# Kernel optimization log

Hardware: AMD Instinct MI355X
Metric: run time of the kernel (lower is better)

## Reference

```python
import jax, jax.numpy as jnp
import numpy as np

BATCH = 256
INPUT_DIM = 64
LEVELS = 100
HV_DIM = 10000


def setup_inputs() -> dict:
    key = jax.random.key(0)
    kx, kb = jax.random.split(key)
    x = jax.random.uniform(kx, (BATCH, INPUT_DIM), dtype=jnp.float32)
    base = jax.random.normal(kb, (INPUT_DIM, LEVELS, HV_DIM), dtype=jnp.float32)
    # buffer is L2-normalized along hv_dim at construction time
    base = base / jnp.linalg.norm(base, axis=-1, keepdims=True)
    return {"x": x, "base_hvs": base}


def reference(x, base_hvs):
    D, L, H = base_hvs.shape
    B = x.shape[0]
    xn = jnp.clip(x * (L - 1), 0.0, float(L - 1))          # [B, D]
    lo = jnp.floor(xn).astype(jnp.int32)                    # [B, D]
    hi = jnp.clip(lo + 1, 0, L - 1)                         # [B, D]
    alpha = xn - lo.astype(x.dtype)                         # [B, D]

    def step(acc, inputs):
        bhv, l, h, a = inputs    # bhv: [L, H], l/h/a: [B]
        hv_low = bhv[l]          # [B, H] gather
        hv_high = bhv[h]         # [B, H] gather
        a = a[:, None]
        return acc + (1.0 - a) * hv_low + a * hv_high, None

    init = jnp.zeros((B, H), dtype=x.dtype)
    encoded, _ = jax.lax.scan(step, init, (base_hvs, lo.T, hi.T, alpha.T))
    return encoded / jnp.linalg.norm(encoded, axis=-1, keepdims=True)
```

## Files before the change

### kernel.cpp

```cpp
#include <hip/hip_runtime.h>
#include <hip/hip_fp16.h>

#define BATCH   256
#define DIMS    64
#define LEVELS  100
#define HVD     10000
#define WH      128
#define NHT     79
#define DSPLIT  8
#define DPER    8
#define TPB     512

__global__ __launch_bounds__(TPB, 4) void encode_kernel(
    const float* __restrict__ x,
    const float* __restrict__ base,
    float* __restrict__ partial)
{
    __shared__ float    s_chunk[LEVELS * WH];
    __shared__ unsigned s_prm[DPER][BATCH];

    const int tid   = threadIdx.x;
    const int w     = tid >> 6;
    const int lane  = tid & 63;
    const int htile = blockIdx.x;
    const int split = blockIdx.y;
    const int h0    = htile * WH;
    const int d0    = split * DPER;
    const int wvalid = (HVD - h0) < WH ? (HVD - h0) : WH;

    for (int i = tid; i < DPER * BATCH; i += TPB) {
        const int dl = i >> 8;
        const int b  = i & 255;
        float xv = x[b * DIMS + d0 + dl];
        float xn = fminf(fmaxf(xv * (float)(LEVELS - 1), 0.0f), (float)(LEVELS - 1));
        float fl = floorf(xn);
        int   lo = (int)fl;
        int   hi = lo < LEVELS - 1 ? lo + 1 : LEVELS - 1;
        unsigned abits = (unsigned)__half_as_ushort(__float2half(xn - fl));
        s_prm[dl][b] = abits | ((unsigned)lo << 16) | ((unsigned)hi << 24);
    }

    const int cix   = lane * 2;
    const int bbase = w * 32;
    const int srow  = lane >> 5;
    const int scol  = (lane & 31) * 4;

    float2 acc[32];
    #pragma unroll
    for (int j = 0; j < 32; ++j) acc[j] = make_float2(0.f, 0.f);

    #pragma unroll 1
    for (int dc = 0; dc < DPER; ++dc) {
        __syncthreads();

        const float* src = base + ((size_t)(d0 + dc) * LEVELS) * (size_t)HVD + h0;
        for (int p = w; p < LEVELS / 2; p += 8) {
            const float* g = src + (size_t)(2 * p + srow) * HVD + scol;
            if (scol < wvalid) {
                __builtin_amdgcn_global_load_lds(
                    (const __attribute__((address_space(1))) unsigned*)g,
                    (__attribute__((address_space(3))) unsigned*)&s_chunk[p * 2 * WH],
                    16, 0, 0);
            }
        }
        __syncthreads();

        #pragma unroll
        for (int jj = 0; jj < 16; ++jj) {
            uint2 pr = *(const uint2*)&s_prm[dc][bbase + 2 * jj];
            {
                const unsigned pk = pr.x;
                const float a  = __half2float(__ushort_as_half((unsigned short)(pk & 0xffffu)));
                const int olo  = (int)((pk >> 16) & 0xffu) * WH;
                const int ohi  = (int)(pk >> 24) * WH;
                float2 vlo = *(const float2*)&s_chunk[olo + cix];
                float2 vhi = *(const float2*)&s_chunk[ohi + cix];
                const float wl = 1.0f - a;
                acc[2 * jj].x += wl * vlo.x + a * vhi.x;
                acc[2 * jj].y += wl * vlo.y + a * vhi.y;
            }
            {
                const unsigned pk = pr.y;
                const float a  = __half2float(__ushort_as_half((unsigned short)(pk & 0xffffu)));
                const int olo  = (int)((pk >> 16) & 0xffu) * WH;
                const int ohi  = (int)(pk >> 24) * WH;
                float2 vlo = *(const float2*)&s_chunk[olo + cix];
                float2 vhi = *(const float2*)&s_chunk[ohi + cix];
                const float wl = 1.0f - a;
                acc[2 * jj + 1].x += wl * vlo.x + a * vhi.x;
                acc[2 * jj + 1].y += wl * vlo.y + a * vhi.y;
            }
        }
    }

    if (cix < wvalid) {
        float* dst = partial + ((size_t)split * BATCH) * (size_t)HVD + h0 + cix;
        #pragma unroll
        for (int j = 0; j < 32; ++j)
            *(float2*)(dst + (size_t)(bbase + j) * HVD) = acc[j];
    }
}

__global__ __launch_bounds__(256) void finish_kernel(
    const float* __restrict__ partial,
    float* __restrict__ out)
{
    const int b   = blockIdx.x;
    const int tid = threadIdx.x;

    float ss = 0.f;
    for (int i = tid; i < HVD / 4; i += 256) {
        float4 s = make_float4(0.f, 0.f, 0.f, 0.f);
        #pragma unroll
        for (int sp = 0; sp < DSPLIT; ++sp) {
            const float4 v = *(const float4*)(partial +
                ((size_t)sp * BATCH + b) * (size_t)HVD + i * 4);
            s.x += v.x; s.y += v.y; s.z += v.z; s.w += v.w;
        }
        *(float4*)(out + (size_t)b * HVD + i * 4) = s;
        ss += s.x * s.x + s.y * s.y + s.z * s.z + s.w * s.w;
    }

    __shared__ float red[256];
    red[tid] = ss;
    __syncthreads();
    #pragma unroll
    for (int s = 128; s > 0; s >>= 1) {
        if (tid < s) red[tid] += red[tid + s];
        __syncthreads();
    }
    const float inv = rsqrtf(red[0]);

    for (int i = tid; i < HVD / 4; i += 256) {
        float4 v = *(float4*)(out + (size_t)b * HVD + i * 4);
        v.x *= inv; v.y *= inv; v.z *= inv; v.w *= inv;
        *(float4*)(out + (size_t)b * HVD + i * 4) = v;
    }
}

extern "C" void kernel_launch(void* const* d_in, const int* in_sizes, int n_in,
                              void* d_out, int out_size, void* d_ws, size_t ws_size,
                              hipStream_t stream)
{
    const float* x    = (const float*)d_in[0];
    const float* base = (const float*)d_in[1];
    float*       out  = (float*)d_out;
    float*       part = (float*)d_ws;

    dim3 grid(NHT, DSPLIT);
    encode_kernel<<<grid, TPB, 0, stream>>>(x, base, part);
    finish_kernel<<<BATCH, 256, 0, stream>>>(part, out);
}
```

Measured before the change: 393.1 us.

## Store partials as bf16, precompute byte-offset params, widen LDS reads to float4

A separate setup kernel now computes the per-(dim,batch) lo/hi byte offsets and fp32 alpha once, and the encoder reads them from global memory instead of rebuilding them in shared memory in every block. Each lane now handles four columns for half as many batch rows, so each LDS read is a float4 (two batches per wave), and the per-split partial sums are written as bf16. This halves both the partial write traffic and the read traffic in the finish kernel. It costs an extra kernel launch and loses precision in the partial sums to bf16 rounding before the final reduction.

```diff
diff --git a/kernel.cpp b/kernel.cpp
--- a/kernel.cpp
+++ b/kernel.cpp
@@ -1,5 +1,5 @@
 #include <hip/hip_runtime.h>
-#include <hip/hip_fp16.h>
+#include <hip/hip_bf16.h>
 
 #define BATCH   256
 #define DIMS    64
@@ -11,13 +11,38 @@
 #define DPER    8
 #define TPB     512
 
+typedef unsigned int  uint;
+typedef unsigned short ushort;
+
+#define PRM_OFF_BYTES (DSPLIT * BATCH * HVD * 2)
+
+static __device__ __forceinline__ ushort f2bf(float f) {
+    __hip_bfloat16 h = __float2bfloat16(f);
+    return *reinterpret_cast<ushort*>(&h);
+}
+
+__global__ __launch_bounds__(256) void setup_kernel(
+    const float* __restrict__ x, uint2* __restrict__ prm)
+{
+    const int i = blockIdx.x * 256 + threadIdx.x;
+    if (i >= DIMS * BATCH) return;
+    const int d = i >> 8;
+    const int b = i & 255;
+    float xv = x[b * DIMS + d];
+    float xn = fminf(fmaxf(xv * (float)(LEVELS - 1), 0.0f), (float)(LEVELS - 1));
+    float fl = floorf(xn);
+    int   lo = (int)fl;
+    int   hi = lo < LEVELS - 1 ? lo + 1 : LEVELS - 1;
+    prm[i] = make_uint2((uint)(lo * WH * 4) | ((uint)(hi * WH * 4) << 16),
+                        __float_as_uint(xn - fl));
+}
+
 __global__ __launch_bounds__(TPB, 4) void encode_kernel(
-    const float* __restrict__ x,
     const float* __restrict__ base,
-    float* __restrict__ partial)
+    const uint2* __restrict__ prm,
+    ushort*      __restrict__ partial)
 {
-    __shared__ float    s_chunk[LEVELS * WH];
-    __shared__ unsigned s_prm[DPER][BATCH];
+    __shared__ float s_chunk[LEVELS * WH];
 
     const int tid   = threadIdx.x;
     const int w     = tid >> 6;
@@ -28,26 +53,19 @@
     const int d0    = split * DPER;
     const int wvalid = (HVD - h0) < WH ? (HVD - h0) : WH;
 
-    for (int i = tid; i < DPER * BATCH; i += TPB) {
-        const int dl = i >> 8;
-        const int b  = i & 255;
-        float xv = x[b * DIMS + d0 + dl];
-        float xn = fminf(fmaxf(xv * (float)(LEVELS - 1), 0.0f), (float)(LEVELS - 1));
-        float fl = floorf(xn);
-        int   lo = (int)fl;
-        int   hi = lo < LEVELS - 1 ? lo + 1 : LEVELS - 1;
-        unsigned abits = (unsigned)__half_as_ushort(__float2half(xn - fl));
-        s_prm[dl][b] = abits | ((unsigned)lo << 16) | ((unsigned)hi << 24);
-    }
+    const int wu    = __builtin_amdgcn_readfirstlane(w);
+    const int bbase = wu * 32;
 
-    const int cix   = lane * 2;
-    const int bbase = w * 32;
-    const int srow  = lane >> 5;
-    const int scol  = (lane & 31) * 4;
+    const int s   = lane >> 5;
+    const int c   = lane & 31;
+    const int cb  = c * 16;
+    const int c4  = c * 4;
+    const int srow = lane >> 5;
+    const int scol = (lane & 31) * 4;
 
-    float2 acc[32];
+    float4 acc[16];
     #pragma unroll
-    for (int j = 0; j < 32; ++j) acc[j] = make_float2(0.f, 0.f);
+    for (int j = 0; j < 16; ++j) acc[j] = make_float4(0.f, 0.f, 0.f, 0.f);
 
     #pragma unroll 1
     for (int dc = 0; dc < DPER; ++dc) {
@@ -58,51 +76,46 @@
             const float* g = src + (size_t)(2 * p + srow) * HVD + scol;
             if (scol < wvalid) {
                 __builtin_amdgcn_global_load_lds(
-                    (const __attribute__((address_space(1))) unsigned*)g,
-                    (__attribute__((address_space(3))) unsigned*)&s_chunk[p * 2 * WH],
+                    (const __attribute__((address_space(1))) uint*)g,
+                    (__attribute__((address_space(3))) uint*)&s_chunk[p * 2 * WH],
                     16, 0, 0);
             }
         }
         __syncthreads();
 
+        const uint2* pr = prm + (size_t)(d0 + dc) * BATCH + bbase;
+
         #pragma unroll
         for (int jj = 0; jj < 16; ++jj) {
-            uint2 pr = *(const uint2*)&s_prm[dc][bbase + 2 * jj];
-            {
-                const unsigned pk = pr.x;
-                const float a  = __half2float(__ushort_as_half((unsigned short)(pk & 0xffffu)));
-                const int olo  = (int)((pk >> 16) & 0xffu) * WH;
-                const int ohi  = (int)(pk >> 24) * WH;
-                float2 vlo = *(const float2*)&s_chunk[olo + cix];
-                float2 vhi = *(const float2*)&s_chunk[ohi + cix];
-                const float wl = 1.0f - a;
-                acc[2 * jj].x += wl * vlo.x + a * vhi.x;
-                acc[2 * jj].y += wl * vlo.y + a * vhi.y;
-            }
-            {
-                const unsigned pk = pr.y;
-                const float a  = __half2float(__ushort_as_half((unsigned short)(pk & 0xffffu)));
-                const int olo  = (int)((pk >> 16) & 0xffu) * WH;
-                const int ohi  = (int)(pk >> 24) * WH;
-                float2 vlo = *(const float2*)&s_chunk[olo + cix];
-                float2 vhi = *(const float2*)&s_chunk[ohi + cix];
-                const float wl = 1.0f - a;
-                acc[2 * jj + 1].x += wl * vlo.x + a * vhi.x;
-                acc[2 * jj + 1].y += wl * vlo.y + a * vhi.y;
-            }
+            const uint4 pq = *(const uint4*)(pr + 2 * jj);
+            const uint  lohi = s ? pq.z : pq.x;
+            const float a    = __uint_as_float(s ? pq.w : pq.y);
+            const int   olo  = (int)(lohi & 0xffffu);
+            const int   ohi  = (int)(lohi >> 16);
+            const float4 vlo = *(const float4*)((const char*)s_chunk + olo + cb);
+            const float4 vhi = *(const float4*)((const char*)s_chunk + ohi + cb);
+            const float wl = 1.0f - a;
+            acc[jj].x += wl * vlo.x + a * vhi.x;
+            acc[jj].y += wl * vlo.y + a * vhi.y;
+            acc[jj].z += wl * vlo.z + a * vhi.z;
+            acc[jj].w += wl * vlo.w + a * vhi.w;
         }
     }
 
-    if (cix < wvalid) {
-        float* dst = partial + ((size_t)split * BATCH) * (size_t)HVD + h0 + cix;
+    if (c4 < wvalid) {
         #pragma unroll
-        for (int j = 0; j < 32; ++j)
-            *(float2*)(dst + (size_t)(bbase + j) * HVD) = acc[j];
+        for (int jj = 0; jj < 16; ++jj) {
+            const int b = bbase + 2 * jj + s;
+            uint2 pk;
+            pk.x = (uint)f2bf(acc[jj].x) | ((uint)f2bf(acc[jj].y) << 16);
+            pk.y = (uint)f2bf(acc[jj].z) | ((uint)f2bf(acc[jj].w) << 16);
+            *(uint2*)(partial + ((size_t)split * BATCH + b) * (size_t)HVD + h0 + c4) = pk;
+        }
     }
 }
 
 __global__ __launch_bounds__(256) void finish_kernel(
-    const float* __restrict__ partial,
+    const ushort* __restrict__ partial,
     float* __restrict__ out)
 {
     const int b   = blockIdx.x;
@@ -110,23 +123,26 @@
 
     float ss = 0.f;
     for (int i = tid; i < HVD / 4; i += 256) {
-        float4 s = make_float4(0.f, 0.f, 0.f, 0.f);
+        float4 sum = make_float4(0.f, 0.f, 0.f, 0.f);
         #pragma unroll
         for (int sp = 0; sp < DSPLIT; ++sp) {
-            const float4 v = *(const float4*)(partial +
+            const uint2 u = *(const uint2*)(partial +
                 ((size_t)sp * BATCH + b) * (size_t)HVD + i * 4);
-            s.x += v.x; s.y += v.y; s.z += v.z; s.w += v.w;
+            sum.x += __uint_as_float(u.x << 16);
+            sum.y += __uint_as_float(u.x & 0xffff0000u);
+            sum.z += __uint_as_float(u.y << 16);
+            sum.w += __uint_as_float(u.y & 0xffff0000u);
         }
-        *(float4*)(out + (size_t)b * HVD + i * 4) = s;
-        ss += s.x * s.x + s.y * s.y + s.z * s.z + s.w * s.w;
+        *(float4*)(out + (size_t)b * HVD + i * 4) = sum;
+        ss += sum.x * sum.x + sum.y * sum.y + sum.z * sum.z + sum.w * sum.w;
     }
 
     __shared__ float red[256];
     red[tid] = ss;
     __syncthreads();
     #pragma unroll
-    for (int s = 128; s > 0; s >>= 1) {
-        if (tid < s) red[tid] += red[tid + s];
+    for (int sh = 128; sh > 0; sh >>= 1) {
+        if (tid < sh) red[tid] += red[tid + sh];
         __syncthreads();
     }
     const float inv = rsqrtf(red[0]);
@@ -145,9 +161,11 @@
     const float* x    = (const float*)d_in[0];
     const float* base = (const float*)d_in[1];
     float*       out  = (float*)d_out;
-    float*       part = (float*)d_ws;
+    ushort*      part = (ushort*)d_ws;
+    uint2*       prm  = (uint2*)((char*)d_ws + PRM_OFF_BYTES);
 
+    setup_kernel<<<DIMS, 256, 0, stream>>>(x, prm);
     dim3 grid(NHT, DSPLIT);
-    encode_kernel<<<grid, TPB, 0, stream>>>(x, base, part);
+    encode_kernel<<<grid, TPB, 0, stream>>>(base, prm, part);
     finish_kernel<<<BATCH, 256, 0, stream>>>(part, out);
 }
```

New measurement: 383.4 us. 1.03x faster.
